# Optimization experiments

Measured on AMD Instinct MI355X. Metric: run time of the kernel, lower is better.

## Reference

```python
import jax, jax.numpy as jnp
import numpy as np

N_NODES = 50000
N_EDGES = 1_600_000
IN_CH = 256
HEADS = 4
OUT_CH = 32


def setup_inputs() -> dict:
    key = jax.random.key(0)
    k1, k2, k3, k4 = jax.random.split(key, 4)
    x = jax.random.normal(k1, (N_NODES, IN_CH), dtype=jnp.float32)
    edge_index = jax.random.randint(k2, (2, N_EDGES), 0, N_NODES, dtype=jnp.int32)
    # xavier-uniform-like init scales
    W = jax.random.uniform(k3, (IN_CH, HEADS * OUT_CH), dtype=jnp.float32,
                           minval=-1.0, maxval=1.0) * np.sqrt(6.0 / (IN_CH + HEADS * OUT_CH))
    attn = jax.random.uniform(k4, (HEADS, 2 * OUT_CH), dtype=jnp.float32,
                              minval=-1.0, maxval=1.0) * np.sqrt(6.0 / (HEADS + 2 * OUT_CH))
    return {"x": x, "edge_index": edge_index, "W": W, "attn": attn}


def reference(x, edge_index, W, attn):
    n = x.shape[0]
    H = attn.shape[0]
    C = attn.shape[1] // 2
    # h = lin(x).view(n, H, C)
    h = (x @ W).reshape(n, H, C)
    row, col = edge_index[0], edge_index[1]
    # (cat([h_row, h_col]) * attn).sum(-1) == h_row.a_src + h_col.a_dst;
    # compute per-node scores then gather per edge (cheaper, same math).
    a_src, a_dst = attn[:, :C], attn[:, C:]
    s_src = jnp.einsum('nhc,hc->nh', h, a_src)  # [n, H]
    s_dst = jnp.einsum('nhc,hc->nh', h, a_dst)  # [n, H]
    alpha = jax.nn.leaky_relu(s_src[row] + s_dst[col], 0.2)  # [E, H]
    # segment softmax over edges grouped by target node `row`
    seg_max = jax.ops.segment_max(alpha, row, num_segments=n)  # [n, H]
    ex = jnp.exp(alpha - seg_max[row])
    denom = jax.ops.segment_sum(ex, row, num_segments=n)  # [n, H]
    alpha_norm = ex / denom[row]  # [E, H]
    # weighted scatter-add of source features (dropout p=0.0 is identity)
    out = jax.ops.segment_sum(alpha_norm[..., None] * h[col], row, num_segments=n)  # [n,H,C]
    return out.mean(axis=1), alpha_norm
```

## Files before the change

kernel.cpp:

```cpp
#include <hip/hip_runtime.h>

#define NNODES 50000
#define NEDGES 1600000
#define IN_CH 256
#define HEADS 4
#define OUT_CH 32
#define HC 128
#define NSB ((NNODES + 255) / 256)
#define NCHUNK 128
#define CE 12500
#define WORDS 25000

typedef unsigned int u32;
typedef unsigned short u16;
typedef short bf16x8 __attribute__((ext_vector_type(8)));
typedef u16 u16x8 __attribute__((ext_vector_type(8)));
typedef float f32x4 __attribute__((ext_vector_type(4)));

__device__ __forceinline__ float b2f(u16 s) { return __uint_as_float(((u32)s) << 16); }
__device__ __forceinline__ u16 f2b(float f) {
  u32 u = __float_as_uint(f);
  u32 r = (u + 0x7FFFu + ((u >> 16) & 1u)) >> 16;
  return (u16)r;
}
__device__ __forceinline__ float lrelu(float v) { return v >= 0.f ? v : 0.2f * v; }

#define NR 16

__global__ __launch_bounds__(256) void k_wprep(const float* __restrict__ W,
                                               u16* __restrict__ wt) {
  int i = blockIdx.x * 256 + threadIdx.x;
  if (i >= IN_CH * HC) return;
  int kk = i & 31;
  int n = (i >> 5) & 127;
  int kt = i >> 12;
  wt[i] = f2b(W[(size_t)(kt * 32 + kk) * HC + n]);
}

__global__ __launch_bounds__(256) void k_gemm(const float* __restrict__ x,
                                              const u16* __restrict__ wt,
                                              const float* __restrict__ attn,
                                              u16* __restrict__ hb,
                                              float* __restrict__ nrec) {
  __shared__ union {
    struct {
      u16 xh[64 * 32];
      u16 xl[64 * 32];
      u16 wh[128 * 32];
    } st;
    float cbuf[64 * 132];
  } L;
  __shared__ float sA[256];
  const int tid = threadIdx.x;
  const int wave = tid >> 6;
  const int lane = tid & 63;
  const int row0 = blockIdx.x * 64;
  sA[tid] = attn[tid];

  f32x4 acc[4][2] = {};
  const int frow = lane & 15;
  const int koff = (lane >> 4) << 4;

  const int sr = tid >> 2;
  const int skc = (tid & 3) << 3;
  const int sgrow = row0 + sr;
  const int sxb = (sr << 6) + (skc << 1);
  const int sxs = sxb ^ ((sr & 7) << 4);

  for (int kt = 0; kt < 8; ++kt) {
    {
      float4 v0 = make_float4(0.f, 0.f, 0.f, 0.f), v1 = v0;
      if (sgrow < NNODES) {
        const float* px = &x[(size_t)sgrow * IN_CH + kt * 32 + skc];
        v0 = *(const float4*)px;
        v1 = *(const float4*)(px + 4);
      }
      float vv[8] = {v0.x, v0.y, v0.z, v0.w, v1.x, v1.y, v1.z, v1.w};
      u16x8 hi, lo;
#pragma unroll
      for (int i = 0; i < 8; ++i) {
        u16 h = f2b(vv[i]);
        hi[i] = h;
        lo[i] = f2b(vv[i] - b2f(h));
      }
      *(u16x8*)((char*)L.st.xh + sxs) = hi;
      *(u16x8*)((char*)L.st.xl + sxs) = lo;
    }
#pragma unroll
    for (int li = 0; li < 2; ++li) {
      int i = tid + (li << 8);
      int col = i >> 2;
      int kb = (i & 3) << 4;
      u16x8 v = *(const u16x8*)((const char*)wt + (((size_t)(kt * 128 + col)) << 6) + kb);
      int sb = ((col << 6) + kb) ^ ((col & 7) << 4);
      *(u16x8*)((char*)L.st.wh + sb) = v;
    }
    __syncthreads();
    bf16x8 ah[4], al[4], bw[2];
#pragma unroll
    for (int mi = 0; mi < 4; ++mi) {
      int r = mi * 16 + frow;
      int sb = ((r << 6) + koff) ^ ((r & 7) << 4);
      ah[mi] = *(bf16x8*)((char*)L.st.xh + sb);
      al[mi] = *(bf16x8*)((char*)L.st.xl + sb);
    }
#pragma unroll
    for (int ni = 0; ni < 2; ++ni) {
      int c = (wave << 5) + ni * 16 + frow;
      int sb = ((c << 6) + koff) ^ ((c & 7) << 4);
      bw[ni] = *(bf16x8*)((char*)L.st.wh + sb);
    }
#pragma unroll
    for (int mi = 0; mi < 4; ++mi)
#pragma unroll
      for (int ni = 0; ni < 2; ++ni) {
        acc[mi][ni] = __builtin_amdgcn_mfma_f32_16x16x32_bf16(ah[mi], bw[ni], acc[mi][ni], 0, 0, 0);
        acc[mi][ni] = __builtin_amdgcn_mfma_f32_16x16x32_bf16(al[mi], bw[ni], acc[mi][ni], 0, 0, 0);
      }
    __syncthreads();
  }

#pragma unroll
  for (int mi = 0; mi < 4; ++mi)
#pragma unroll
    for (int ni = 0; ni < 2; ++ni) {
#pragma unroll
      for (int reg = 0; reg < 4; ++reg) {
        int row = mi * 16 + ((lane >> 4) << 2) + reg;
        int col = (wave << 5) + (ni << 4) + frow;
        L.cbuf[row * 132 + col] = acc[mi][ni][reg];
      }
    }
  __syncthreads();

  const int tc = tid & 31;
  const int tr = tid >> 5;
  const int head = tc >> 3;
  const int cb = (tc & 7) << 2;
  const float4 as4 = *(const float4*)&sA[head * 64 + cb];
  const float4 ad4 = *(const float4*)&sA[head * 64 + 32 + cb];
#pragma unroll
  for (int i = 0; i < 8; ++i) {
    int row = (tr << 3) + i;
    int grow = row0 + row;
    float4 v = *(const float4*)&L.cbuf[row * 132 + (tc << 2)];
    float ps = v.x * as4.x + v.y * as4.y + v.z * as4.z + v.w * as4.w;
    float pd = v.x * ad4.x + v.y * ad4.y + v.z * ad4.z + v.w * ad4.w;
    ps += __shfl_xor(ps, 1); ps += __shfl_xor(ps, 2); ps += __shfl_xor(ps, 4);
    pd += __shfl_xor(pd, 1); pd += __shfl_xor(pd, 2); pd += __shfl_xor(pd, 4);
    if (grow < NNODES) {
      u16 q[4] = {f2b(v.x), f2b(v.y), f2b(v.z), f2b(v.w)};
      *(ushort4*)&hb[(size_t)grow * HC + (tc << 2)] = *(ushort4*)q;
      if ((tc & 7) == 0) {
        nrec[(size_t)grow * NR + head] = ps;
        nrec[(size_t)grow * NR + 4 + head] = pd;
      }
    }
  }
}

__global__ __launch_bounds__(256) void k_chist(const int* __restrict__ rowi,
                                               u32* __restrict__ chunk_hist,
                                               u16* __restrict__ lslot) {
  __shared__ u32 lh[WORDS];
  const int c = blockIdx.x;
  const int tid = threadIdx.x;
  for (int i = tid; i < WORDS; i += 256) lh[i] = 0;
  __syncthreads();
  const int base = c * CE;
  for (int i = tid; i < CE; i += 256) {
    int e = base + i;
    int r = rowi[e];
    u32 sh = (u32)(r & 1) << 4;
    u32 old = atomicAdd(&lh[r >> 1], 1u << sh);
    lslot[e] = (u16)((old >> sh) & 0xFFFFu);
  }
  __syncthreads();
  u32* dst = chunk_hist + (size_t)c * WORDS;
  for (int i = tid; i < WORDS; i += 256) dst[i] = lh[i];
}

__global__ __launch_bounds__(256) void k_cscan(u32* __restrict__ chunk_hist,
                                               int* __restrict__ counts) {
  __shared__ u32 tile[NCHUNK][64];
  const int w0 = blockIdx.x * 64;
  const int tid = threadIdx.x;
  for (int i = tid; i < NCHUNK * 64; i += 256) {
    int c = i >> 6, wl = i & 63;
    int w = w0 + wl;
    tile[c][wl] = (w < WORDS) ? chunk_hist[(size_t)c * WORDS + w] : 0u;
  }
  __syncthreads();
  if (tid < 64) {
    u32 slo = 0, shi = 0;
    for (int c = 0; c < NCHUNK; ++c) {
      u32 v = tile[c][tid];
      tile[c][tid] = slo | (shi << 16);
      slo += v & 0xFFFFu;
      shi += v >> 16;
    }
    int w = w0 + tid;
    if (w < WORDS) {
      int r = w << 1;
      if (r < NNODES) counts[r] = (int)slo;
      if (r + 1 < NNODES) counts[r + 1] = (int)shi;
    }
  }
  __syncthreads();
  for (int i = tid; i < NCHUNK * 64; i += 256) {
    int c = i >> 6, wl = i & 63;
    int w = w0 + wl;
    if (w < WORDS) chunk_hist[(size_t)c * WORDS + w] = tile[c][wl];
  }
}

__global__ __launch_bounds__(256) void k_scan1(const int* __restrict__ counts,
                                               int* __restrict__ bsum) {
  int i = blockIdx.x * 256 + threadIdx.x;
  int v = (i < NNODES) ? counts[i] : 0;
#pragma unroll
  for (int m = 1; m < 64; m <<= 1) v += __shfl_xor(v, m);
  __shared__ int ws[4];
  if ((threadIdx.x & 63) == 0) ws[threadIdx.x >> 6] = v;
  __syncthreads();
  if (threadIdx.x == 0) bsum[blockIdx.x] = ws[0] + ws[1] + ws[2] + ws[3];
}

__global__ __launch_bounds__(256) void k_scan2(const int* __restrict__ bsum,
                                               int* __restrict__ boff) {
  __shared__ int s[256];
  int t = threadIdx.x;
  int v = (t < NSB) ? bsum[t] : 0;
  s[t] = v;
  __syncthreads();
  for (int off = 1; off < 256; off <<= 1) {
    int u = (t >= off) ? s[t - off] : 0;
    __syncthreads();
    s[t] += u;
    __syncthreads();
  }
  boff[t] = s[t] - v;
}

__global__ __launch_bounds__(256) void k_scan3(const int* __restrict__ counts,
                                               const int* __restrict__ boff,
                                               int* __restrict__ row_ptr) {
  __shared__ int s[256];
  int t = threadIdx.x;
  int i = blockIdx.x * 256 + t;
  int v = (i < NNODES) ? counts[i] : 0;
  s[t] = v;
  __syncthreads();
  for (int off = 1; off < 256; off <<= 1) {
    int u = (t >= off) ? s[t - off] : 0;
    __syncthreads();
    s[t] += u;
    __syncthreads();
  }
  if (i < NNODES) row_ptr[i] = boff[blockIdx.x] + s[t] - v;
  if (i == 0) row_ptr[NNODES] = NEDGES;
}

__global__ void k_scatter(const int* __restrict__ rowi, const int* __restrict__ coli,
                          const int* __restrict__ row_ptr,
                          const u32* __restrict__ chunk_hist,
                          const u16* __restrict__ lslot,
                          u16* __restrict__ col_csr) {
  int e = blockIdx.x * 256 + threadIdx.x;
  if (e >= NEDGES) return;
  int r = rowi[e];
  int c = e / CE;
  u32 word = chunk_hist[(size_t)c * WORDS + (r >> 1)];
  int off = (int)((word >> ((u32)(r & 1) << 4)) & 0xFFFFu);
  int pos = row_ptr[r] + off + (int)lslot[e];
  col_csr[pos] = (u16)coli[e];
}

__global__ __launch_bounds__(256) void k_softmax(const u16* __restrict__ col_csr,
                                                 const int* __restrict__ row_ptr,
                                                 float* __restrict__ nrec,
                                                 u16* __restrict__ an16) {
  const int wid = threadIdx.x >> 6;
  const int lane = threadIdx.x & 63;
  const int r = blockIdx.x * 4 + wid;
  if (r >= NNODES) return;
  const int p0 = row_ptr[r], p1 = row_ptr[r + 1];
  const int deg = p1 - p0;
  if (deg == 0) return;
  const float4 ss = *(const float4*)&nrec[(size_t)r * NR];
  const float NEG = -3.0e38f;

  if (deg <= 64) {
    float4 al = make_float4(NEG, NEG, NEG, NEG);
    if (lane < deg) {
      int c = col_csr[p0 + lane];
      float4 sd = *(const float4*)&nrec[(size_t)c * NR + 4];
      al.x = lrelu(ss.x + sd.x);
      al.y = lrelu(ss.y + sd.y);
      al.z = lrelu(ss.z + sd.z);
      al.w = lrelu(ss.w + sd.w);
    }
    float4 mx = al;
#pragma unroll
    for (int m = 1; m < 64; m <<= 1) {
      mx.x = fmaxf(mx.x, __shfl_xor(mx.x, m));
      mx.y = fmaxf(mx.y, __shfl_xor(mx.y, m));
      mx.z = fmaxf(mx.z, __shfl_xor(mx.z, m));
      mx.w = fmaxf(mx.w, __shfl_xor(mx.w, m));
    }
    float4 ex = make_float4(0.f, 0.f, 0.f, 0.f);
    if (lane < deg) {
      ex.x = __expf(al.x - mx.x);
      ex.y = __expf(al.y - mx.y);
      ex.z = __expf(al.z - mx.z);
      ex.w = __expf(al.w - mx.w);
    }
    float4 sm = ex;
#pragma unroll
    for (int m = 1; m < 64; m <<= 1) {
      sm.x += __shfl_xor(sm.x, m);
      sm.y += __shfl_xor(sm.y, m);
      sm.z += __shfl_xor(sm.z, m);
      sm.w += __shfl_xor(sm.w, m);
    }
    float4 rd = make_float4(1.f / sm.x, 1.f / sm.y, 1.f / sm.z, 1.f / sm.w);
    if (lane == 0) {
      *(float4*)&nrec[(size_t)r * NR + 8] = mx;
      *(float4*)&nrec[(size_t)r * NR + 12] = rd;
    }
    if (lane < deg) {
      u16 q[4] = {f2b(ex.x * rd.x), f2b(ex.y * rd.y), f2b(ex.z * rd.z), f2b(ex.w * rd.w)};
      *(ushort4*)&an16[(size_t)(p0 + lane) * 4] = *(ushort4*)q;
    }
  } else {
    float4 mx = make_float4(NEG, NEG, NEG, NEG);
    for (int p = p0 + lane; p < p1; p += 64) {
      int c = col_csr[p];
      float4 sd = *(const float4*)&nrec[(size_t)c * NR + 4];
      mx.x = fmaxf(mx.x, lrelu(ss.x + sd.x));
      mx.y = fmaxf(mx.y, lrelu(ss.y + sd.y));
      mx.z = fmaxf(mx.z, lrelu(ss.z + sd.z));
      mx.w = fmaxf(mx.w, lrelu(ss.w + sd.w));
    }
#pragma unroll
    for (int m = 1; m < 64; m <<= 1) {
      mx.x = fmaxf(mx.x, __shfl_xor(mx.x, m));
      mx.y = fmaxf(mx.y, __shfl_xor(mx.y, m));
      mx.z = fmaxf(mx.z, __shfl_xor(mx.z, m));
      mx.w = fmaxf(mx.w, __shfl_xor(mx.w, m));
    }
    float4 sm = make_float4(0.f, 0.f, 0.f, 0.f);
    for (int p = p0 + lane; p < p1; p += 64) {
      int c = col_csr[p];
      float4 sd = *(const float4*)&nrec[(size_t)c * NR + 4];
      sm.x += __expf(lrelu(ss.x + sd.x) - mx.x);
      sm.y += __expf(lrelu(ss.y + sd.y) - mx.y);
      sm.z += __expf(lrelu(ss.z + sd.z) - mx.z);
      sm.w += __expf(lrelu(ss.w + sd.w) - mx.w);
    }
#pragma unroll
    for (int m = 1; m < 64; m <<= 1) {
      sm.x += __shfl_xor(sm.x, m);
      sm.y += __shfl_xor(sm.y, m);
      sm.z += __shfl_xor(sm.z, m);
      sm.w += __shfl_xor(sm.w, m);
    }
    float4 rd = make_float4(1.f / sm.x, 1.f / sm.y, 1.f / sm.z, 1.f / sm.w);
    if (lane == 0) {
      *(float4*)&nrec[(size_t)r * NR + 8] = mx;
      *(float4*)&nrec[(size_t)r * NR + 12] = rd;
    }
    for (int p = p0 + lane; p < p1; p += 64) {
      int c = col_csr[p];
      float4 sd = *(const float4*)&nrec[(size_t)c * NR + 4];
      float4 ex;
      ex.x = __expf(lrelu(ss.x + sd.x) - mx.x) * rd.x;
      ex.y = __expf(lrelu(ss.y + sd.y) - mx.y) * rd.y;
      ex.z = __expf(lrelu(ss.z + sd.z) - mx.z) * rd.z;
      ex.w = __expf(lrelu(ss.w + sd.w) - mx.w) * rd.w;
      u16 q[4] = {f2b(ex.x), f2b(ex.y), f2b(ex.z), f2b(ex.w)};
      *(ushort4*)&an16[(size_t)p * 4] = *(ushort4*)q;
    }
  }
}

__global__ void k_alphaf(const int* __restrict__ rowi, const int* __restrict__ coli,
                         const float* __restrict__ nrec,
                         float* __restrict__ alpha_out) {
  int e = blockIdx.x * 256 + threadIdx.x;
  if (e >= NEDGES) return;
  int r = rowi[e], c = coli[e];
  const float* nr = &nrec[(size_t)r * NR];
  float4 ss = *(const float4*)(nr);
  float4 m4 = *(const float4*)(nr + 8);
  float4 rd = *(const float4*)(nr + 12);
  float4 sd = *(const float4*)&nrec[(size_t)c * NR + 4];
  float4 an;
  an.x = __expf(lrelu(ss.x + sd.x) - m4.x) * rd.x;
  an.y = __expf(lrelu(ss.y + sd.y) - m4.y) * rd.y;
  an.z = __expf(lrelu(ss.z + sd.z) - m4.z) * rd.z;
  an.w = __expf(lrelu(ss.w + sd.w) - m4.w) * rd.w;
  *(float4*)&alpha_out[(size_t)e * 4] = an;
}

__global__ __launch_bounds__(256) void k_aggr(const u16* __restrict__ col_csr,
                                              const int* __restrict__ row_ptr,
                                              const u16* __restrict__ an16,
                                              const u16* __restrict__ hb,
                                              float* __restrict__ out_mean) {
  const int wid = threadIdx.x >> 6;
  const int lane = threadIdx.x & 63;
  const int r = blockIdx.x * 4 + wid;
  if (r >= NNODES) return;
  const int p0 = row_ptr[r], p1 = row_ptr[r + 1];
  const int half = lane >> 5;
  const int sl = lane & 31;
  const int hd = sl >> 3;
  const int boff = sl << 3;
  float a0 = 0.f, a1 = 0.f, a2 = 0.f, a3 = 0.f;

  int p = p0;
  for (; p + 16 <= p1; p += 16) {
    int cs[8];
    float wv[8];
    u32 h0[8], h1[8];
#pragma unroll
    for (int i = 0; i < 8; ++i) {
      int idx = p + (i << 1) + half;
      cs[i] = col_csr[idx];
      wv[i] = b2f(an16[(size_t)idx * 4 + hd]);
    }
#pragma unroll
    for (int i = 0; i < 8; ++i) {
      const u32* hp = (const u32*)((const char*)hb + ((size_t)cs[i] << 8) + boff);
      h0[i] = hp[0];
      h1[i] = hp[1];
    }
#pragma unroll
    for (int i = 0; i < 8; ++i) {
      a0 += wv[i] * __uint_as_float(h0[i] << 16);
      a1 += wv[i] * __uint_as_float(h0[i] & 0xFFFF0000u);
      a2 += wv[i] * __uint_as_float(h1[i] << 16);
      a3 += wv[i] * __uint_as_float(h1[i] & 0xFFFF0000u);
    }
  }
  for (; p < p1; p += 2) {
    int idx = p + half;
    bool act = idx < p1;
    int c = act ? (int)col_csr[idx] : 0;
    float w = act ? b2f(an16[(size_t)idx * 4 + hd]) : 0.f;
    const u32* hp = (const u32*)((const char*)hb + ((size_t)c << 8) + boff);
    u32 x0 = hp[0], x1 = hp[1];
    a0 += w * __uint_as_float(x0 << 16);
    a1 += w * __uint_as_float(x0 & 0xFFFF0000u);
    a2 += w * __uint_as_float(x1 << 16);
    a3 += w * __uint_as_float(x1 & 0xFFFF0000u);
  }
  a0 += __shfl_xor(a0, 32); a1 += __shfl_xor(a1, 32);
  a2 += __shfl_xor(a2, 32); a3 += __shfl_xor(a3, 32);
  a0 += __shfl_xor(a0, 8);  a1 += __shfl_xor(a1, 8);
  a2 += __shfl_xor(a2, 8);  a3 += __shfl_xor(a3, 8);
  a0 += __shfl_xor(a0, 16); a1 += __shfl_xor(a1, 16);
  a2 += __shfl_xor(a2, 16); a3 += __shfl_xor(a3, 16);
  if (lane < 8) {
    float4 o = make_float4(a0 * 0.25f, a1 * 0.25f, a2 * 0.25f, a3 * 0.25f);
    *(float4*)&out_mean[(size_t)r * 32 + (lane << 2)] = o;
  }
}

extern "C" void kernel_launch(void* const* d_in, const int* in_sizes, int n_in,
                              void* d_out, int out_size, void* d_ws, size_t ws_size,
                              hipStream_t stream) {
  const float* x = (const float*)d_in[0];
  const int* ei = (const int*)d_in[1];
  const float* W = (const float*)d_in[2];
  const float* attn = (const float*)d_in[3];
  const int* rowi = ei;
  const int* coli = ei + NEDGES;

  float* out_mean = (float*)d_out;
  float* alpha_out = (float*)d_out + (size_t)NNODES * 32;

  char* w = (char*)d_ws;
  u16* hb = (u16*)w;          w += (size_t)NNODES * HC * 2;
  u16* an16 = (u16*)w;        w += (size_t)NEDGES * 4 * 2;
  float* nrec = (float*)w;    w += (size_t)NNODES * NR * 4;
  int* counts = (int*)w;      w += (size_t)NNODES * 4;
  int* bsum = (int*)w;        w += (size_t)256 * 4;
  int* boff = (int*)w;        w += (size_t)256 * 4;
  int* row_ptr = (int*)w;     w += (size_t)50016 * 4;
  u16* lslot = (u16*)w;       w += (size_t)NEDGES * 2;
  u16* col_csr = (u16*)w;     w += (size_t)NEDGES * 2;
  u32* chunk_hist = (u32*)w;  w += (size_t)NCHUNK * WORDS * 4;
  u16* wt = (u16*)w;          w += (size_t)IN_CH * HC * 2;

  k_wprep<<<(IN_CH * HC + 255) / 256, 256, 0, stream>>>(W, wt);
  k_gemm<<<(NNODES + 63) / 64, 256, 0, stream>>>(x, wt, attn, hb, nrec);
  k_chist<<<NCHUNK, 256, 0, stream>>>(rowi, chunk_hist, lslot);
  k_cscan<<<(WORDS + 63) / 64, 256, 0, stream>>>(chunk_hist, counts);
  k_scan1<<<NSB, 256, 0, stream>>>(counts, bsum);
  k_scan2<<<1, 256, 0, stream>>>(bsum, boff);
  k_scan3<<<NSB, 256, 0, stream>>>(counts, boff, row_ptr);
  k_scatter<<<(NEDGES + 255) / 256, 256, 0, stream>>>(rowi, coli, row_ptr, chunk_hist, lslot, col_csr);
  k_softmax<<<(NNODES + 3) / 4, 256, 0, stream>>>(col_csr, row_ptr, nrec, an16);
  k_alphaf<<<(NEDGES + 255) / 256, 256, 0, stream>>>(rowi, coli, nrec, alpha_out);
  k_aggr<<<(NNODES + 3) / 4, 256, 0, stream>>>(col_csr, row_ptr, an16, hb, out_mean);
}
```

Measured before the change: 230.1 us.

## Split aggregation per head with head-major feature and weight layouts

The projected features and normalized attention weights are stored head-major, so each head's 32-channel slice of all nodes forms a compact 3.2MB array. Aggregation launches one block per node group and head, so each wave handles 8 edges at a time for a single head, and per-head partial sums are added by a new reduction kernel. The aim is better cache locality in the random gathers, since each head's slice fits in L2. The cost is four times as many aggregation blocks, an extra kernel launch, a partial-output buffer aliased over dead scratch space, and scattered 2-byte weight stores in softmax.

```diff
diff --git a/kernel.cpp b/kernel.cpp
--- a/kernel.cpp
+++ b/kernel.cpp
@@ -150,7 +150,7 @@
     pd += __shfl_xor(pd, 1); pd += __shfl_xor(pd, 2); pd += __shfl_xor(pd, 4);
     if (grow < NNODES) {
       u16 q[4] = {f2b(v.x), f2b(v.y), f2b(v.z), f2b(v.w)};
-      *(ushort4*)&hb[(size_t)grow * HC + (tc << 2)] = *(ushort4*)q;
+      *(ushort4*)&hb[((size_t)head * NNODES + grow) * 32 + cb] = *(ushort4*)q;
       if ((tc & 7) == 0) {
         nrec[(size_t)grow * NR + head] = ps;
         nrec[(size_t)grow * NR + 4 + head] = pd;
@@ -279,7 +279,7 @@
 __global__ __launch_bounds__(256) void k_softmax(const u16* __restrict__ col_csr,
                                                  const int* __restrict__ row_ptr,
                                                  float* __restrict__ nrec,
-                                                 u16* __restrict__ an16) {
+                                                 u16* __restrict__ an_h) {
   const int wid = threadIdx.x >> 6;
   const int lane = threadIdx.x & 63;
   const int r = blockIdx.x * 4 + wid;
@@ -329,8 +329,11 @@
       *(float4*)&nrec[(size_t)r * NR + 12] = rd;
     }
     if (lane < deg) {
-      u16 q[4] = {f2b(ex.x * rd.x), f2b(ex.y * rd.y), f2b(ex.z * rd.z), f2b(ex.w * rd.w)};
-      *(ushort4*)&an16[(size_t)(p0 + lane) * 4] = *(ushort4*)q;
+      int pos = p0 + lane;
+      an_h[pos] = f2b(ex.x * rd.x);
+      an_h[(size_t)NEDGES + pos] = f2b(ex.y * rd.y);
+      an_h[(size_t)NEDGES * 2 + pos] = f2b(ex.z * rd.z);
+      an_h[(size_t)NEDGES * 3 + pos] = f2b(ex.w * rd.w);
     }
   } else {
     float4 mx = make_float4(NEG, NEG, NEG, NEG);
@@ -378,8 +381,10 @@
       ex.y = __expf(lrelu(ss.y + sd.y) - mx.y) * rd.y;
       ex.z = __expf(lrelu(ss.z + sd.z) - mx.z) * rd.z;
       ex.w = __expf(lrelu(ss.w + sd.w) - mx.w) * rd.w;
-      u16 q[4] = {f2b(ex.x), f2b(ex.y), f2b(ex.z), f2b(ex.w)};
-      *(ushort4*)&an16[(size_t)p * 4] = *(ushort4*)q;
+      an_h[p] = f2b(ex.x);
+      an_h[(size_t)NEDGES + p] = f2b(ex.y);
+      an_h[(size_t)NEDGES * 2 + p] = f2b(ex.z);
+      an_h[(size_t)NEDGES * 3 + p] = f2b(ex.w);
     }
   }
 }
@@ -405,67 +410,80 @@
 
 __global__ __launch_bounds__(256) void k_aggr(const u16* __restrict__ col_csr,
                                               const int* __restrict__ row_ptr,
-                                              const u16* __restrict__ an16,
+                                              const u16* __restrict__ an_h,
                                               const u16* __restrict__ hb,
-                                              float* __restrict__ out_mean) {
+                                              float* __restrict__ out_part) {
   const int wid = threadIdx.x >> 6;
   const int lane = threadIdx.x & 63;
-  const int r = blockIdx.x * 4 + wid;
+  const int head = blockIdx.x & 3;
+  const int r = (blockIdx.x >> 2) * 4 + wid;
   if (r >= NNODES) return;
   const int p0 = row_ptr[r], p1 = row_ptr[r + 1];
-  const int half = lane >> 5;
-  const int sl = lane & 31;
-  const int hd = sl >> 3;
-  const int boff = sl << 3;
+  const int eslot = lane >> 3;
+  const int cl = lane & 7;
+  const u16* an_p = an_h + (size_t)head * NEDGES;
+  const u16* hb_p = hb + (size_t)head * NNODES * 32;
   float a0 = 0.f, a1 = 0.f, a2 = 0.f, a3 = 0.f;
 
   int p = p0;
-  for (; p + 16 <= p1; p += 16) {
-    int cs[8];
-    float wv[8];
-    u32 h0[8], h1[8];
-#pragma unroll
-    for (int i = 0; i < 8; ++i) {
-      int idx = p + (i << 1) + half;
+  for (; p + 32 <= p1; p += 32) {
+    int cs[4];
+    float wv[4];
+    u32 h0[4], h1[4];
+#pragma unroll
+    for (int i = 0; i < 4; ++i) {
+      int idx = p + (i << 3) + eslot;
       cs[i] = col_csr[idx];
-      wv[i] = b2f(an16[(size_t)idx * 4 + hd]);
-    }
-#pragma unroll
-    for (int i = 0; i < 8; ++i) {
-      const u32* hp = (const u32*)((const char*)hb + ((size_t)cs[i] << 8) + boff);
+      wv[i] = b2f(an_p[idx]);
+    }
+#pragma unroll
+    for (int i = 0; i < 4; ++i) {
+      const u32* hp = (const u32*)(hb_p + ((size_t)cs[i] << 5) + (cl << 2));
       h0[i] = hp[0];
       h1[i] = hp[1];
     }
 #pragma unroll
-    for (int i = 0; i < 8; ++i) {
+    for (int i = 0; i < 4; ++i) {
       a0 += wv[i] * __uint_as_float(h0[i] << 16);
       a1 += wv[i] * __uint_as_float(h0[i] & 0xFFFF0000u);
       a2 += wv[i] * __uint_as_float(h1[i] << 16);
       a3 += wv[i] * __uint_as_float(h1[i] & 0xFFFF0000u);
     }
   }
-  for (; p < p1; p += 2) {
-    int idx = p + half;
+  for (; p < p1; p += 8) {
+    int idx = p + eslot;
     bool act = idx < p1;
     int c = act ? (int)col_csr[idx] : 0;
-    float w = act ? b2f(an16[(size_t)idx * 4 + hd]) : 0.f;
-    const u32* hp = (const u32*)((const char*)hb + ((size_t)c << 8) + boff);
+    float w = act ? b2f(an_p[idx]) : 0.f;
+    const u32* hp = (const u32*)(hb_p + ((size_t)c << 5) + (cl << 2));
     u32 x0 = hp[0], x1 = hp[1];
     a0 += w * __uint_as_float(x0 << 16);
     a1 += w * __uint_as_float(x0 & 0xFFFF0000u);
     a2 += w * __uint_as_float(x1 << 16);
     a3 += w * __uint_as_float(x1 & 0xFFFF0000u);
   }
-  a0 += __shfl_xor(a0, 32); a1 += __shfl_xor(a1, 32);
-  a2 += __shfl_xor(a2, 32); a3 += __shfl_xor(a3, 32);
   a0 += __shfl_xor(a0, 8);  a1 += __shfl_xor(a1, 8);
   a2 += __shfl_xor(a2, 8);  a3 += __shfl_xor(a3, 8);
   a0 += __shfl_xor(a0, 16); a1 += __shfl_xor(a1, 16);
   a2 += __shfl_xor(a2, 16); a3 += __shfl_xor(a3, 16);
+  a0 += __shfl_xor(a0, 32); a1 += __shfl_xor(a1, 32);
+  a2 += __shfl_xor(a2, 32); a3 += __shfl_xor(a3, 32);
   if (lane < 8) {
     float4 o = make_float4(a0 * 0.25f, a1 * 0.25f, a2 * 0.25f, a3 * 0.25f);
-    *(float4*)&out_mean[(size_t)r * 32 + (lane << 2)] = o;
-  }
+    *(float4*)&out_part[(((size_t)head * NNODES + r) << 5) + (lane << 2)] = o;
+  }
+}
+
+__global__ void k_redu(const float* __restrict__ out_part,
+                       float* __restrict__ out_mean) {
+  int i = blockIdx.x * 256 + threadIdx.x;
+  if (i >= NNODES * 8) return;
+  const float4* p0 = (const float4*)out_part;
+  const size_t ps = (size_t)NNODES * 8;
+  float4 a = p0[i], b = p0[i + ps], c = p0[i + 2 * ps], d = p0[i + 3 * ps];
+  float4 o = make_float4(a.x + b.x + c.x + d.x, a.y + b.y + c.y + d.y,
+                         a.z + b.z + c.z + d.z, a.w + b.w + c.w + d.w);
+  ((float4*)out_mean)[i] = o;
 }
 
 extern "C" void kernel_launch(void* const* d_in, const int* in_sizes, int n_in,
@@ -483,16 +501,18 @@
 
   char* w = (char*)d_ws;
   u16* hb = (u16*)w;          w += (size_t)NNODES * HC * 2;
-  u16* an16 = (u16*)w;        w += (size_t)NEDGES * 4 * 2;
+  u16* an_h = (u16*)w;        w += (size_t)NEDGES * 4 * 2;
   float* nrec = (float*)w;    w += (size_t)NNODES * NR * 4;
   int* counts = (int*)w;      w += (size_t)NNODES * 4;
   int* bsum = (int*)w;        w += (size_t)256 * 4;
   int* boff = (int*)w;        w += (size_t)256 * 4;
   int* row_ptr = (int*)w;     w += (size_t)50016 * 4;
-  u16* lslot = (u16*)w;       w += (size_t)NEDGES * 2;
   u16* col_csr = (u16*)w;     w += (size_t)NEDGES * 2;
-  u32* chunk_hist = (u32*)w;  w += (size_t)NCHUNK * WORDS * 4;
-  u16* wt = (u16*)w;          w += (size_t)IN_CH * HC * 2;
+  char* regionA = w;
+  u16* lslot = (u16*)regionA;
+  u32* chunk_hist = (u32*)(regionA + (size_t)NEDGES * 2);
+  u16* wt = (u16*)(regionA + (size_t)NEDGES * 2 + (size_t)NCHUNK * WORDS * 4);
+  float* out_part = (float*)regionA;
 
   k_wprep<<<(IN_CH * HC + 255) / 256, 256, 0, stream>>>(W, wt);
   k_gemm<<<(NNODES + 63) / 64, 256, 0, stream>>>(x, wt, attn, hb, nrec);
@@ -502,7 +522,8 @@
   k_scan2<<<1, 256, 0, stream>>>(bsum, boff);
   k_scan3<<<NSB, 256, 0, stream>>>(counts, boff, row_ptr);
   k_scatter<<<(NEDGES + 255) / 256, 256, 0, stream>>>(rowi, coli, row_ptr, chunk_hist, lslot, col_csr);
-  k_softmax<<<(NNODES + 3) / 4, 256, 0, stream>>>(col_csr, row_ptr, nrec, an16);
+  k_softmax<<<(NNODES + 3) / 4, 256, 0, stream>>>(col_csr, row_ptr, nrec, an_h);
   k_alphaf<<<(NEDGES + 255) / 256, 256, 0, stream>>>(rowi, coli, nrec, alpha_out);
-  k_aggr<<<(NNODES + 3) / 4, 256, 0, stream>>>(col_csr, row_ptr, an16, hb, out_mean);
-}
+  k_aggr<<<((NNODES + 3) / 4) * 4, 256, 0, stream>>>(col_csr, row_ptr, an_h, hb, out_part);
+  k_redu<<<(NNODES * 8 + 255) / 256, 256, 0, stream>>>(out_part, out_mean);
+}
```

Result: slower. 271.6 us (+18.1%).
